# Optimization experiments

Hardware: AMD Instinct MI355X
Metric: run time of the kernel (lower is better)

Reference implementation:

```python
import jax, jax.numpy as jnp
import numpy as np

MARGIN = 0.3
PD_EPS = 1e-6  # torch.nn.functional.pairwise_distance default eps (added to the diff)


def setup_inputs() -> dict:
    key = jax.random.key(0)
    k1, k2 = jax.random.split(key)
    n, d = 8192, 128
    inputs = jax.random.normal(k1, (n, d), dtype=jnp.float32)
    positive = jax.random.normal(k2, (n, d), dtype=jnp.float32)
    return {"inputs": inputs, "positive": positive}


def reference(inputs, positive):
    # Pairwise squared Euclidean distances: ||xi||^2 + ||xj||^2 - 2 xi.xj  -> [n, n]
    sq = jnp.sum(inputs * inputs, axis=1, keepdims=True)  # [n, 1]
    dist = sq + sq.T - 2.0 * (inputs @ inputs.T)
    dist = jnp.sqrt(jnp.clip(dist, 1e-12, None))

    # Original: dist[i].argsort()[4] -> 5th-nearest (index 0 is self at ~0 distance).
    # Equivalent, avoiding full per-row sort: top-5 smallest distances.
    _, idx = jax.lax.top_k(-dist, 5)  # idx: [n, 5], ascending by distance
    negative = inputs[idx[:, 4]]  # hard negatives, [n, d]

    # TripletMarginLoss(margin=0.3, p=2): pairwise_distance adds eps to the diff.
    d_ap = jnp.linalg.norm(inputs - positive + PD_EPS, axis=1)
    d_an = jnp.linalg.norm(inputs - negative + PD_EPS, axis=1)
    return jnp.mean(jnp.maximum(d_ap - d_an + MARGIN, 0.0))
```

## Files before the change

### kernel.cpp

```cpp
#include <hip/hip_runtime.h>

#define NN 8192
#define DD 128
#define CH 16
#define CPC (NN / CH)
#define TILES (CPC / 64)
#define NPART 64

typedef __bf16 bf16x8 __attribute__((ext_vector_type(8)));
typedef float f32x4 __attribute__((ext_vector_type(4)));

#define PACK_INIT __uint_as_float(0x7F7FFFFFu)

static __device__ __forceinline__ float packsi(float s, unsigned idx) {
  return __uint_as_float((__float_as_uint(s) & 0xFFFFE000u) | idx);
}

#define NET4(S0, S1, S2, S3, v)                                                \
  {                                                                            \
    float v_ = (v), o0 = S0, o1 = S1, o2 = S2;                                 \
    S0 = fminf(o0, v_);                                                        \
    S1 = __builtin_amdgcn_fmed3f(v_, o0, o1);                                  \
    S2 = __builtin_amdgcn_fmed3f(v_, o1, o2);                                  \
    S3 = __builtin_amdgcn_fmed3f(v_, o2, S3);                                  \
  }
#define NET5(S0, S1, S2, S3, S4, v)                                            \
  {                                                                            \
    float v_ = (v), o0 = S0, o1 = S1, o2 = S2, o3 = S3;                        \
    S0 = fminf(o0, v_);                                                        \
    S1 = __builtin_amdgcn_fmed3f(v_, o0, o1);                                  \
    S2 = __builtin_amdgcn_fmed3f(v_, o1, o2);                                  \
    S3 = __builtin_amdgcn_fmed3f(v_, o2, o3);                                  \
    S4 = __builtin_amdgcn_fmed3f(v_, o3, S4);                                  \
  }

static __device__ __forceinline__ unsigned short f2bf(float f) {
  unsigned u = __float_as_uint(f);
  u += 0x7FFFu + ((u >> 16) & 1u);
  return (unsigned short)(u >> 16);
}

__global__ __launch_bounds__(256) void prep_kernel(const float* __restrict__ x,
                                                   unsigned short* __restrict__ xb,
                                                   float* __restrict__ sq,
                                                   float* __restrict__ partial) {
  const int wave = threadIdx.x >> 6, lane = threadIdx.x & 63;
  const int row = blockIdx.x * 4 + wave;
  const float2 v = ((const float2*)(x + (size_t)row * DD))[lane];
  float ss = v.x * v.x + v.y * v.y;
#pragma unroll
  for (int off = 32; off; off >>= 1) ss += __shfl_down(ss, off);
  if (lane == 0) sq[row] = ss;
  unsigned packed = (unsigned)f2bf(v.x) | ((unsigned)f2bf(v.y) << 16);
  ((unsigned*)(xb + (size_t)row * DD))[lane] = packed;
  if (blockIdx.x == 0 && threadIdx.x < NPART) partial[threadIdx.x] = 0.0f;
}

__global__ __launch_bounds__(256, 2) void dist_topk_kernel(
    const unsigned short* __restrict__ xb, const float* __restrict__ sq,
    float* __restrict__ pscore) {
  const int t = threadIdx.x;
  const int wave = t >> 6, lane = t & 63;
  const int lrow = lane & 15, lquad = lane >> 4;
  const int rowBase = blockIdx.x * 256;
  const int chunk = blockIdx.y;
  const int j0 = chunk * CPC;
  const bool hasDiag = ((blockIdx.x >> 1) == (int)blockIdx.y);

  __shared__ unsigned short colsB[2][64 * DD];
  __shared__ float sqs[2][64];

  const int r0 = rowBase + wave * 64 + lrow;
  const unsigned short* ap0 = xb + (size_t)(r0)*DD + lquad * 8;
  const unsigned short* ap1 = xb + (size_t)(r0 + 16) * DD + lquad * 8;
  const unsigned short* ap2 = xb + (size_t)(r0 + 32) * DD + lquad * 8;
  const unsigned short* ap3 = xb + (size_t)(r0 + 48) * DD + lquad * 8;
  bf16x8 a00 = *(const bf16x8*)(ap0), a01 = *(const bf16x8*)(ap0 + 32),
         a02 = *(const bf16x8*)(ap0 + 64), a03 = *(const bf16x8*)(ap0 + 96);
  bf16x8 a10 = *(const bf16x8*)(ap1), a11 = *(const bf16x8*)(ap1 + 32),
         a12 = *(const bf16x8*)(ap1 + 64), a13 = *(const bf16x8*)(ap1 + 96);
  bf16x8 a20 = *(const bf16x8*)(ap2), a21 = *(const bf16x8*)(ap2 + 32),
         a22 = *(const bf16x8*)(ap2 + 64), a23 = *(const bf16x8*)(ap2 + 96);
  bf16x8 a30 = *(const bf16x8*)(ap3), a31 = *(const bf16x8*)(ap3 + 32),
         a32 = *(const bf16x8*)(ap3 + 64), a33 = *(const bf16x8*)(ap3 + 96);

  float q00 = PACK_INIT, q01 = PACK_INIT, q02 = PACK_INIT, q03 = PACK_INIT,
        q04 = PACK_INIT;
  float q10 = PACK_INIT, q11 = PACK_INIT, q12 = PACK_INIT, q13 = PACK_INIT,
        q14 = PACK_INIT;
  float q20 = PACK_INIT, q21 = PACK_INIT, q22 = PACK_INIT, q23 = PACK_INIT,
        q24 = PACK_INIT;
  float q30 = PACK_INIT, q31 = PACK_INIT, q32 = PACK_INIT, q33 = PACK_INIT,
        q34 = PACK_INIT;

  const int sr = t >> 4, sch = t & 15;
  const int dst0 = (sr << 4) | (sch ^ (sr & 15));

  const float4* srcv = (const float4*)(xb + (size_t)j0 * DD);
  float4 g0 = srcv[t], g1 = srcv[t + 256], g2 = srcv[t + 512], g3 = srcv[t + 768];
  float sqv = 0.0f;
  if (t < 64) sqv = sq[j0 + t];

#define KBODY(INSROW)                                                          \
  for (int it = 0; it < TILES; ++it) {                                         \
    const int jt = j0 + it * 64;                                               \
    const int cur = it & 1;                                                    \
    {                                                                          \
      float4* dstv = (float4*)colsB[cur];                                      \
      dstv[dst0] = g0;                                                         \
      dstv[dst0 + 256] = g1;                                                   \
      dstv[dst0 + 512] = g2;                                                   \
      dstv[dst0 + 768] = g3;                                                   \
      if (t < 64) sqs[cur][t] = sqv;                                           \
    }                                                                          \
    if (it + 1 < TILES) {                                                      \
      const float4* nsrc = (const float4*)(xb + (size_t)(jt + 64) * DD);       \
      g0 = nsrc[t]; g1 = nsrc[t + 256]; g2 = nsrc[t + 512]; g3 = nsrc[t + 768];\
      if (t < 64) sqv = sq[jt + 64 + t];                                       \
    }                                                                          \
    __syncthreads();                                                           \
    _Pragma("unroll")                                                          \
    for (int ct = 0; ct < 4; ++ct) {                                           \
      const unsigned short* bb = &colsB[cur][(ct * 16 + lrow) * DD];           \
      bf16x8 b0 = *(const bf16x8*)(bb + (((0 + lquad) ^ lrow) << 3));          \
      bf16x8 b1 = *(const bf16x8*)(bb + (((4 + lquad) ^ lrow) << 3));          \
      bf16x8 b2 = *(const bf16x8*)(bb + (((8 + lquad) ^ lrow) << 3));          \
      bf16x8 b3 = *(const bf16x8*)(bb + (((12 + lquad) ^ lrow) << 3));         \
      f32x4 ac0 = {0.f, 0.f, 0.f, 0.f}, ac1 = {0.f, 0.f, 0.f, 0.f};           \
      f32x4 ac2 = {0.f, 0.f, 0.f, 0.f}, ac3 = {0.f, 0.f, 0.f, 0.f};           \
      ac0 = __builtin_amdgcn_mfma_f32_16x16x32_bf16(b0, a00, ac0, 0, 0, 0);    \
      ac1 = __builtin_amdgcn_mfma_f32_16x16x32_bf16(b0, a10, ac1, 0, 0, 0);    \
      ac2 = __builtin_amdgcn_mfma_f32_16x16x32_bf16(b0, a20, ac2, 0, 0, 0);    \
      ac3 = __builtin_amdgcn_mfma_f32_16x16x32_bf16(b0, a30, ac3, 0, 0, 0);    \
      ac0 = __builtin_amdgcn_mfma_f32_16x16x32_bf16(b1, a01, ac0, 0, 0, 0);    \
      ac1 = __builtin_amdgcn_mfma_f32_16x16x32_bf16(b1, a11, ac1, 0, 0, 0);    \
      ac2 = __builtin_amdgcn_mfma_f32_16x16x32_bf16(b1, a21, ac2, 0, 0, 0);    \
      ac3 = __builtin_amdgcn_mfma_f32_16x16x32_bf16(b1, a31, ac3, 0, 0, 0);    \
      ac0 = __builtin_amdgcn_mfma_f32_16x16x32_bf16(b2, a02, ac0, 0, 0, 0);    \
      ac1 = __builtin_amdgcn_mfma_f32_16x16x32_bf16(b2, a12, ac1, 0, 0, 0);    \
      ac2 = __builtin_amdgcn_mfma_f32_16x16x32_bf16(b2, a22, ac2, 0, 0, 0);    \
      ac3 = __builtin_amdgcn_mfma_f32_16x16x32_bf16(b2, a32, ac3, 0, 0, 0);    \
      ac0 = __builtin_amdgcn_mfma_f32_16x16x32_bf16(b3, a03, ac0, 0, 0, 0);    \
      ac1 = __builtin_amdgcn_mfma_f32_16x16x32_bf16(b3, a13, ac1, 0, 0, 0);    \
      ac2 = __builtin_amdgcn_mfma_f32_16x16x32_bf16(b3, a23, ac2, 0, 0, 0);    \
      ac3 = __builtin_amdgcn_mfma_f32_16x16x32_bf16(b3, a33, ac3, 0, 0, 0);    \
      const f32x4 sq4 = *(const f32x4*)&sqs[cur][ct * 16 + lquad * 4];         \
      const unsigned colb = (unsigned)(jt + ct * 16 + lquad * 4);              \
      _Pragma("unroll")                                                        \
      for (int r = 0; r < 4; ++r) {                                            \
        INSROW(0, packsi(fmaf(-2.0f, ac0[r], sq4[r]), colb + r));              \
        INSROW(1, packsi(fmaf(-2.0f, ac1[r], sq4[r]), colb + r));              \
        INSROW(2, packsi(fmaf(-2.0f, ac2[r], sq4[r]), colb + r));              \
        INSROW(3, packsi(fmaf(-2.0f, ac3[r], sq4[r]), colb + r));              \
      }                                                                        \
    }                                                                          \
  }

#define INS4(G, V) NET4(q##G##0, q##G##1, q##G##2, q##G##3, (V))
#define INS5(G, V) NET5(q##G##0, q##G##1, q##G##2, q##G##3, q##G##4, (V))

  if (hasDiag) {
    KBODY(INS5)
  } else {
    KBODY(INS4)
  }
#undef KBODY

#define MERGE4(G, M)                                                           \
  {                                                                            \
    float o0 = __shfl_xor(q##G##0, M), o1 = __shfl_xor(q##G##1, M),            \
          o2 = __shfl_xor(q##G##2, M), o3 = __shfl_xor(q##G##3, M);            \
    NET4(q##G##0, q##G##1, q##G##2, q##G##3, o0);                              \
    NET4(q##G##0, q##G##1, q##G##2, q##G##3, o1);                              \
    NET4(q##G##0, q##G##1, q##G##2, q##G##3, o2);                              \
    NET4(q##G##0, q##G##1, q##G##2, q##G##3, o3);                              \
  }
#define MERGE5(G, M)                                                           \
  {                                                                            \
    float o0 = __shfl_xor(q##G##0, M), o1 = __shfl_xor(q##G##1, M),            \
          o2 = __shfl_xor(q##G##2, M), o3 = __shfl_xor(q##G##3, M),            \
          o4 = __shfl_xor(q##G##4, M);                                         \
    NET5(q##G##0, q##G##1, q##G##2, q##G##3, q##G##4, o0);                     \
    NET5(q##G##0, q##G##1, q##G##2, q##G##3, q##G##4, o1);                     \
    NET5(q##G##0, q##G##1, q##G##2, q##G##3, q##G##4, o2);                     \
    NET5(q##G##0, q##G##1, q##G##2, q##G##3, q##G##4, o3);                     \
    NET5(q##G##0, q##G##1, q##G##2, q##G##3, q##G##4, o4);                     \
  }
  if (hasDiag) {
    MERGE5(0, 16) MERGE5(1, 16) MERGE5(2, 16) MERGE5(3, 16)
    MERGE5(0, 32) MERGE5(1, 32) MERGE5(2, 32) MERGE5(3, 32)
  } else {
    MERGE4(0, 16) MERGE4(1, 16) MERGE4(2, 16) MERGE4(3, 16)
    MERGE4(0, 32) MERGE4(1, 32) MERGE4(2, 32) MERGE4(3, 32)
  }

  if (lquad == 0) {
    float* b0p = pscore + (size_t)(r0)*80 + chunk * 5;
    b0p[0] = q00; b0p[1] = q01; b0p[2] = q02; b0p[3] = q03; b0p[4] = q04;
    float* b1p = pscore + (size_t)(r0 + 16) * 80 + chunk * 5;
    b1p[0] = q10; b1p[1] = q11; b1p[2] = q12; b1p[3] = q13; b1p[4] = q14;
    float* b2p = pscore + (size_t)(r0 + 32) * 80 + chunk * 5;
    b2p[0] = q20; b2p[1] = q21; b2p[2] = q22; b2p[3] = q23; b2p[4] = q24;
    float* b3p = pscore + (size_t)(r0 + 48) * 80 + chunk * 5;
    b3p[0] = q30; b3p[1] = q31; b3p[2] = q32; b3p[3] = q33; b3p[4] = q34;
  }
}

__global__ __launch_bounds__(256) void final_kernel(const float* __restrict__ x,
                                                    const float* __restrict__ pos,
                                                    const float* __restrict__ pscore,
                                                    float* __restrict__ partial) {
  const int wave = threadIdx.x >> 6, lane = threadIdx.x & 63;
  const int row = blockIdx.x * 4 + wave;

  float q0 = PACK_INIT, q1 = PACK_INIT, q2 = PACK_INIT, q3 = PACK_INIT,
        q4 = PACK_INIT;
  if (lane < CH) {
    const float* b = pscore + (size_t)row * 80 + lane * 5;
    q0 = b[0]; q1 = b[1]; q2 = b[2]; q3 = b[3]; q4 = b[4];
  }
#pragma unroll
  for (int m = 1; m < CH; m <<= 1) {
    float o0 = __shfl_xor(q0, m), o1 = __shfl_xor(q1, m), o2 = __shfl_xor(q2, m),
          o3 = __shfl_xor(q3, m), o4 = __shfl_xor(q4, m);
    NET5(q0, q1, q2, q3, q4, o0);
    NET5(q0, q1, q2, q3, q4, o1);
    NET5(q0, q1, q2, q3, q4, o2);
    NET5(q0, q1, q2, q3, q4, o3);
    NET5(q0, q1, q2, q3, q4, o4);
  }
  const int nidx = (int)(__float_as_uint(__shfl(q4, 0)) & 0x1FFFu);

  const float2 xv  = ((const float2*)(x   + (size_t)row  * DD))[lane];
  const float2 pv  = ((const float2*)(pos + (size_t)row  * DD))[lane];
  const float2 nvv = ((const float2*)(x   + (size_t)nidx * DD))[lane];
  float a0 = xv.x - pv.x + 1e-6f, a1 = xv.y - pv.y + 1e-6f;
  float b0 = xv.x - nvv.x + 1e-6f, b1 = xv.y - nvv.y + 1e-6f;
  float dap = a0 * a0 + a1 * a1;
  float dan = b0 * b0 + b1 * b1;
#pragma unroll
  for (int off = 32; off; off >>= 1) {
    dap += __shfl_down(dap, off);
    dan += __shfl_down(dan, off);
  }
  __shared__ float hs[4];
  if (lane == 0) hs[wave] = fmaxf(sqrtf(dap) - sqrtf(dan) + 0.3f, 0.0f);
  __syncthreads();
  if (threadIdx.x == 0) {
    float s = hs[0] + hs[1] + hs[2] + hs[3];
    atomicAdd(&partial[blockIdx.x & (NPART - 1)], s);
  }
}

__global__ __launch_bounds__(64) void reduce_kernel(const float* __restrict__ partial,
                                                    float* __restrict__ out) {
  float v = partial[threadIdx.x];
#pragma unroll
  for (int off = 32; off; off >>= 1) v += __shfl_down(v, off);
  if (threadIdx.x == 0) out[0] = v * (1.0f / 8192.0f);
}

extern "C" void kernel_launch(void* const* d_in, const int* in_sizes, int n_in,
                              void* d_out, int out_size, void* d_ws, size_t ws_size,
                              hipStream_t stream) {
  const float* x   = (const float*)d_in[0];
  const float* pos = (const float*)d_in[1];
  float* out = (float*)d_out;

  char* w = (char*)d_ws;
  unsigned short* xb = (unsigned short*)w;
  float* sq = (float*)(w + (size_t)NN * DD * 2);
  float* pscore = (float*)(w + (size_t)NN * DD * 2 + (size_t)NN * 4);
  float* partial = (float*)(w + (size_t)NN * DD * 2 + (size_t)NN * 4 +
                            (size_t)NN * 80 * 4);

  prep_kernel<<<NN / 4, 256, 0, stream>>>(x, xb, sq, partial);
  dist_topk_kernel<<<dim3(NN / 256, CH), 256, 0, stream>>>(xb, sq, pscore);
  final_kernel<<<NN / 4, 256, 0, stream>>>(x, pos, pscore, partial);
  reduce_kernel<<<1, 64, 0, stream>>>(partial, out);
}
```

Baseline: 106.2 us.

## Stage two column tiles per barrier and fold final reduction into last block

The distance/top-k kernel now loads and stores two 64-column tiles per iteration into a four-slot LDS ring. This halves the number of __syncthreads and issues larger prefetch batches. Separately, the standalone reduce kernel is removed: the last finishing block of final_kernel, found with an atomic counter, sums the partials and writes the mean. In exchange, LDS use doubles to about 64KB per block, which may lower occupancy under launch_bounds(256,2), and prefetch registers double.

```diff
diff --git a/kernel.cpp b/kernel.cpp
--- a/kernel.cpp
+++ b/kernel.cpp
@@ -43,7 +43,8 @@
 __global__ __launch_bounds__(256) void prep_kernel(const float* __restrict__ x,
                                                    unsigned short* __restrict__ xb,
                                                    float* __restrict__ sq,
-                                                   float* __restrict__ partial) {
+                                                   float* __restrict__ partial,
+                                                   int* __restrict__ done) {
   const int wave = threadIdx.x >> 6, lane = threadIdx.x & 63;
   const int row = blockIdx.x * 4 + wave;
   const float2 v = ((const float2*)(x + (size_t)row * DD))[lane];
@@ -53,7 +54,10 @@
   if (lane == 0) sq[row] = ss;
   unsigned packed = (unsigned)f2bf(v.x) | ((unsigned)f2bf(v.y) << 16);
   ((unsigned*)(xb + (size_t)row * DD))[lane] = packed;
-  if (blockIdx.x == 0 && threadIdx.x < NPART) partial[threadIdx.x] = 0.0f;
+  if (blockIdx.x == 0) {
+    if (threadIdx.x < NPART) partial[threadIdx.x] = 0.0f;
+    if (threadIdx.x == 0) done[0] = 0;
+  }
 }
 
 __global__ __launch_bounds__(256, 2) void dist_topk_kernel(
@@ -67,8 +71,8 @@
   const int j0 = chunk * CPC;
   const bool hasDiag = ((blockIdx.x >> 1) == (int)blockIdx.y);
 
-  __shared__ unsigned short colsB[2][64 * DD];
-  __shared__ float sqs[2][64];
+  __shared__ unsigned short colsB[4][64 * DD];
+  __shared__ float sqs[4][64];
 
   const int r0 = rowBase + wave * 64 + lrow;
   const unsigned short* ap0 = xb + (size_t)(r0)*DD + lquad * 8;
@@ -96,32 +100,17 @@
   const int sr = t >> 4, sch = t & 15;
   const int dst0 = (sr << 4) | (sch ^ (sr & 15));
 
-  const float4* srcv = (const float4*)(xb + (size_t)j0 * DD);
-  float4 g0 = srcv[t], g1 = srcv[t + 256], g2 = srcv[t + 512], g3 = srcv[t + 768];
-  float sqv = 0.0f;
-  if (t < 64) sqv = sq[j0 + t];
-
-#define KBODY(INSROW)                                                          \
-  for (int it = 0; it < TILES; ++it) {                                         \
-    const int jt = j0 + it * 64;                                               \
-    const int cur = it & 1;                                                    \
-    {                                                                          \
-      float4* dstv = (float4*)colsB[cur];                                      \
-      dstv[dst0] = g0;                                                         \
-      dstv[dst0 + 256] = g1;                                                   \
-      dstv[dst0 + 512] = g2;                                                   \
-      dstv[dst0 + 768] = g3;                                                   \
-      if (t < 64) sqs[cur][t] = sqv;                                           \
-    }                                                                          \
-    if (it + 1 < TILES) {                                                      \
-      const float4* nsrc = (const float4*)(xb + (size_t)(jt + 64) * DD);       \
-      g0 = nsrc[t]; g1 = nsrc[t + 256]; g2 = nsrc[t + 512]; g3 = nsrc[t + 768];\
-      if (t < 64) sqv = sq[jt + 64 + t];                                       \
-    }                                                                          \
-    __syncthreads();                                                           \
+  const float4* s0v = (const float4*)(xb + (size_t)j0 * DD);
+  const float4* s1v = (const float4*)(xb + (size_t)(j0 + 64) * DD);
+  float4 g0 = s0v[t], g1 = s0v[t + 256], g2 = s0v[t + 512], g3 = s0v[t + 768];
+  float4 h0 = s1v[t], h1 = s1v[t + 256], h2 = s1v[t + 512], h3 = s1v[t + 768];
+  float sqg = 0.0f, sqh = 0.0f;
+  if (t < 64) { sqg = sq[j0 + t]; sqh = sq[j0 + 64 + t]; }
+
+#define COMPUTE_TILE(CUR, JT, INSROW)                                          \
     _Pragma("unroll")                                                          \
     for (int ct = 0; ct < 4; ++ct) {                                           \
-      const unsigned short* bb = &colsB[cur][(ct * 16 + lrow) * DD];           \
+      const unsigned short* bb = &colsB[CUR][(ct * 16 + lrow) * DD];           \
       bf16x8 b0 = *(const bf16x8*)(bb + (((0 + lquad) ^ lrow) << 3));          \
       bf16x8 b1 = *(const bf16x8*)(bb + (((4 + lquad) ^ lrow) << 3));          \
       bf16x8 b2 = *(const bf16x8*)(bb + (((8 + lquad) ^ lrow) << 3));          \
@@ -144,8 +133,8 @@
       ac1 = __builtin_amdgcn_mfma_f32_16x16x32_bf16(b3, a13, ac1, 0, 0, 0);    \
       ac2 = __builtin_amdgcn_mfma_f32_16x16x32_bf16(b3, a23, ac2, 0, 0, 0);    \
       ac3 = __builtin_amdgcn_mfma_f32_16x16x32_bf16(b3, a33, ac3, 0, 0, 0);    \
-      const f32x4 sq4 = *(const f32x4*)&sqs[cur][ct * 16 + lquad * 4];         \
-      const unsigned colb = (unsigned)(jt + ct * 16 + lquad * 4);              \
+      const f32x4 sq4 = *(const f32x4*)&sqs[CUR][ct * 16 + lquad * 4];         \
+      const unsigned colb = (unsigned)((JT) + ct * 16 + lquad * 4);            \
       _Pragma("unroll")                                                        \
       for (int r = 0; r < 4; ++r) {                                            \
         INSROW(0, packsi(fmaf(-2.0f, ac0[r], sq4[r]), colb + r));              \
@@ -153,7 +142,31 @@
         INSROW(2, packsi(fmaf(-2.0f, ac2[r], sq4[r]), colb + r));              \
         INSROW(3, packsi(fmaf(-2.0f, ac3[r], sq4[r]), colb + r));              \
       }                                                                        \
+    }
+
+#define KBODY(INSROW)                                                          \
+  for (int it = 0; it < TILES; it += 2) {                                      \
+    const int jt = j0 + it * 64;                                               \
+    const int c0 = it & 3, c1 = (it & 3) | 1;                                  \
+    {                                                                          \
+      float4* d0 = (float4*)colsB[c0];                                         \
+      d0[dst0] = g0; d0[dst0 + 256] = g1;                                      \
+      d0[dst0 + 512] = g2; d0[dst0 + 768] = g3;                                \
+      float4* d1 = (float4*)colsB[c1];                                         \
+      d1[dst0] = h0; d1[dst0 + 256] = h1;                                      \
+      d1[dst0 + 512] = h2; d1[dst0 + 768] = h3;                                \
+      if (t < 64) { sqs[c0][t] = sqg; sqs[c1][t] = sqh; }                      \
     }                                                                          \
+    __syncthreads();                                                           \
+    if (it + 2 < TILES) {                                                      \
+      const float4* n0 = (const float4*)(xb + (size_t)(jt + 128) * DD);        \
+      const float4* n1 = (const float4*)(xb + (size_t)(jt + 192) * DD);        \
+      g0 = n0[t]; g1 = n0[t + 256]; g2 = n0[t + 512]; g3 = n0[t + 768];        \
+      h0 = n1[t]; h1 = n1[t + 256]; h2 = n1[t + 512]; h3 = n1[t + 768];        \
+      if (t < 64) { sqg = sq[jt + 128 + t]; sqh = sq[jt + 192 + t]; }          \
+    }                                                                          \
+    COMPUTE_TILE(c0, jt, INSROW)                                               \
+    COMPUTE_TILE(c1, jt + 64, INSROW)                                          \
   }
 
 #define INS4(G, V) NET4(q##G##0, q##G##1, q##G##2, q##G##3, (V))
@@ -165,6 +178,7 @@
     KBODY(INS4)
   }
 #undef KBODY
+#undef COMPUTE_TILE
 
 #define MERGE4(G, M)                                                           \
   {                                                                            \
@@ -209,7 +223,9 @@
 __global__ __launch_bounds__(256) void final_kernel(const float* __restrict__ x,
                                                     const float* __restrict__ pos,
                                                     const float* __restrict__ pscore,
-                                                    float* __restrict__ partial) {
+                                                    float* __restrict__ partial,
+                                                    int* __restrict__ done,
+                                                    float* __restrict__ out) {
   const int wave = threadIdx.x >> 6, lane = threadIdx.x & 63;
   const int row = blockIdx.x * 4 + wave;
 
@@ -244,20 +260,23 @@
     dan += __shfl_down(dan, off);
   }
   __shared__ float hs[4];
+  __shared__ int amlast;
   if (lane == 0) hs[wave] = fmaxf(sqrtf(dap) - sqrtf(dan) + 0.3f, 0.0f);
   __syncthreads();
   if (threadIdx.x == 0) {
     float s = hs[0] + hs[1] + hs[2] + hs[3];
     atomicAdd(&partial[blockIdx.x & (NPART - 1)], s);
-  }
-}
-
-__global__ __launch_bounds__(64) void reduce_kernel(const float* __restrict__ partial,
-                                                    float* __restrict__ out) {
-  float v = partial[threadIdx.x];
+    __threadfence();
+    int v = atomicAdd(done, 1);
+    amlast = (v == (int)gridDim.x - 1);
+  }
+  __syncthreads();
+  if (amlast && threadIdx.x < NPART) {
+    float v = atomicAdd(&partial[threadIdx.x], 0.0f);
 #pragma unroll
-  for (int off = 32; off; off >>= 1) v += __shfl_down(v, off);
-  if (threadIdx.x == 0) out[0] = v * (1.0f / 8192.0f);
+    for (int off = 32; off; off >>= 1) v += __shfl_down(v, off);
+    if (threadIdx.x == 0) out[0] = v * (1.0f / 8192.0f);
+  }
 }
 
 extern "C" void kernel_launch(void* const* d_in, const int* in_sizes, int n_in,
@@ -271,11 +290,11 @@
   unsigned short* xb = (unsigned short*)w;
   float* sq = (float*)(w + (size_t)NN * DD * 2);
   float* pscore = (float*)(w + (size_t)NN * DD * 2 + (size_t)NN * 4);
-  float* partial = (float*)(w + (size_t)NN * DD * 2 + (size_t)NN * 4 +
-                            (size_t)NN * 80 * 4);
-
-  prep_kernel<<<NN / 4, 256, 0, stream>>>(x, xb, sq, partial);
+  char* w3 = w + (size_t)NN * DD * 2 + (size_t)NN * 4 + (size_t)NN * 80 * 4;
+  float* partial = (float*)w3;
+  int* done = (int*)(w3 + NPART * 4);
+
+  prep_kernel<<<NN / 4, 256, 0, stream>>>(x, xb, sq, partial, done);
   dist_topk_kernel<<<dim3(NN / 256, CH), 256, 0, stream>>>(xb, sq, pscore);
-  final_kernel<<<NN / 4, 256, 0, stream>>>(x, pos, pscore, partial);
-  reduce_kernel<<<1, 64, 0, stream>>>(partial, out);
-}
+  final_kernel<<<NN / 4, 256, 0, stream>>>(x, pos, pscore, partial, done, out);
+}
```

After: 131.4 us. 1.24x slower.
